# Performance work log

Hardware: AMD Instinct MI355X
Metric: run time of the kernel (lower is better)

Reference implementation:

```python
import jax, jax.numpy as jnp
import numpy as np

B, S, T = 32, 512, 2048
D_TXT, D_MEL = 256, 80


def conv1d(x, w, b, pad):
    # x: (B, C_in, L), w: (C_out, C_in, K)
    y = jax.lax.conv_general_dilated(x, w, window_strides=(1,), padding=[(pad, pad)],
                                     dimension_numbers=('NCH', 'OIH', 'NCH'))
    return y + b[None, :, None]


def text_encoder(x, tw1, tb1, tw2, tb2):
    h = jax.nn.relu(conv1d(x, tw1, tb1, 1))
    return conv1d(h, tw2, tb2, 0)


def mel_encoder(x, mw1, mb1, mw2, mb2, mw3, mb3):
    h = jax.nn.leaky_relu(conv1d(x, mw1, mb1, 1), 0.01)
    h = jax.nn.leaky_relu(conv1d(h, mw2, mb2, 1), 0.01)
    return conv1d(h, mw3, mb3, 0)


def cdist(a, b):
    # a: (B,S,D), b: (B,T,D) -> (B,S,T) euclidean (torch.cdist p=2)
    d2 = (jnp.sum(a * a, -1)[:, :, None] + jnp.sum(b * b, -1)[:, None, :]
          - 2.0 * jnp.einsum('bsd,btd->bst', a, b))
    return jnp.sqrt(jnp.maximum(d2, 1e-12))


def maximum_path(value, mask):
    # Glow-TTS monotonic alignment search. value, mask: (B,S,T) float.
    b, s, t = value.shape
    neg_inf = jnp.float32(-jnp.inf)
    val = (value * mask).transpose(2, 0, 1)  # (T,B,S)
    x_range = jnp.arange(s)

    def fwd_step(v, jc):
        j, col = jc
        v0 = jnp.concatenate([jnp.full((b, 1), neg_inf, v.dtype), v[:, :-1]], axis=1)
        keep = v >= v0  # True: best predecessor is same text index
        v_max = jnp.where(keep, v, v0)
        v_new = jnp.where(x_range[None, :] <= j, v_max + col, neg_inf)
        return v_new, keep

    _, dirs = jax.lax.scan(fwd_step, jnp.zeros((b, s), value.dtype), (jnp.arange(t), val))
    direction = jnp.where(mask.astype(bool), dirs.transpose(1, 2, 0), True).astype(jnp.int32)

    index0 = jnp.sum(mask[:, :, 0], axis=1).astype(jnp.int32) - 1

    def bwd_step(index, dcol):
        row = (jnp.arange(s)[None, :] == index[:, None]).astype(value.dtype)
        d = jnp.take_along_axis(dcol, index[:, None], axis=1)[:, 0]
        return index + d - 1, row

    dcols_rev = jnp.flip(direction, axis=2).transpose(2, 0, 1)  # (T,B,S)
    _, rows = jax.lax.scan(bwd_step, index0, dcols_rev)
    path = jnp.flip(rows, axis=0).transpose(1, 2, 0)  # (B,S,T)
    return path * mask


def setup_inputs() -> dict:
    key = jax.random.key(0)
    ks = jax.random.split(key, 16)
    text = jax.random.normal(ks[0], (B, S, D_TXT), jnp.float32)
    mel = jax.random.normal(ks[1], (B, T, D_MEL), jnp.float32)
    src_len = jax.random.randint(ks[2], (B,), S // 2, S + 1).astype(jnp.int32)
    mel_len = jax.random.randint(ks[3], (B,), T // 2, T + 1).astype(jnp.int32)
    src_mask = jnp.arange(S)[None, :] >= src_len[:, None]   # True = pad
    mel_mask = jnp.arange(T)[None, :] >= mel_len[:, None]
    attn_mask = jnp.zeros((B, S, T), bool)  # unused in forward
    sc = 0.05
    params = dict(
        tw1=jax.random.normal(ks[4], (512, 256, 3)) * sc, tb1=jnp.zeros((512,)),
        tw2=jax.random.normal(ks[5], (80, 512, 1)) * sc, tb2=jnp.zeros((80,)),
        mw1=jax.random.normal(ks[6], (160, 80, 3)) * sc, mb1=jnp.zeros((160,)),
        mw2=jax.random.normal(ks[7], (80, 160, 3)) * sc, mb2=jnp.zeros((80,)),
        mw3=jax.random.normal(ks[8], (80, 80, 1)) * sc, mb3=jnp.zeros((80,)),
    )
    return dict(text=text, mel=mel, src_len=src_len, mel_len=mel_len,
                src_mask=src_mask, mel_mask=mel_mask, attn_mask=attn_mask, **params)


def reference(text, mel, src_len, mel_len, src_mask, mel_mask, attn_mask,
              tw1, tb1, tw2, tb2, mw1, mb1, mw2, mb2, mw3, mb3):
    text_emb = text_encoder(text.transpose(0, 2, 1), tw1, tb1, tw2, tb2).transpose(0, 2, 1)
    mel_emb = mel_encoder(mel.transpose(0, 2, 1), mw1, mb1, mw2, mb2, mw3, mb3).transpose(0, 2, 1)
    text_emb = jnp.where(src_mask[:, :, None], 0.0, text_emb)
    mel_emb = jnp.where(mel_mask[:, :, None], 0.0, mel_emb)
    dist = cdist(text_emb, mel_emb)  # (B,S,T)
    mask1 = jnp.arange(S)[None, :] < src_len[:, None]
    mask2 = jnp.arange(T)[None, :] < mel_len[:, None]
    mask_ST = mask1[:, :, None] & mask2[:, None, :]
    rev = ~mask_ST
    logits = jnp.where(rev, jnp.float32(-1e9), -dist)
    soft_A = jax.nn.softmax(logits, axis=1)  # softmax over text dim
    soft_A = jnp.where(rev, 0.0, soft_A)
    hard_A = maximum_path(soft_A, mask_ST.astype(soft_A.dtype))
    return soft_A, hard_A, rev
```

## Files before the change

kernel.cpp:

```cpp
#include <hip/hip_runtime.h>
#include <hip/hip_bf16.h>
#include <cstdint>

constexpr int NB_ = 32;
constexpr int NS_ = 512;
constexpr int NT_ = 2048;
constexpr int DMEL = 80;

constexpr size_t P = 134217728ull;
constexpr size_t PO_TE   = 0ull;
constexpr size_t PO_ME   = 5242880ull;
constexpr size_t PO_NA   = 26214400ull;
constexpr size_t PO_NB   = 26279936ull;
constexpr size_t PO_W1   = 27066368ull;
constexpr size_t PO_W2   = 28639232ull;
constexpr size_t PO_W3   = 28803072ull;
constexpr size_t PO_W4   = 28956672ull;
constexpr size_t PO_W5   = 29110272ull;
constexpr size_t PO_DIR  = 29139968ull;
constexpr size_t FULL_NEED = P + 33334528ull;

__global__ void k_wtrans(const float* __restrict__ w, float* __restrict__ wT,
                         int CO, int CI, int KW, int total) {
  int id = blockIdx.x * 256 + threadIdx.x;
  if (id >= total) return;
  int co = id % CO;
  int rest = id / CO;
  int ci = rest % CI;
  int tap = rest / CI;
  wT[id] = w[(co * CI + ci) * KW + tap];
}

template <int CIN, int COUT, int NTILE, int NR, int KC, int LOG2L, int ACT,
          bool MASK, bool NORM>
__global__ __launch_bounds__(256) void k_conv(const float* __restrict__ x,
                                              const float* __restrict__ wT,
                                              const float* __restrict__ bias,
                                              float* __restrict__ y,
                                              const int* __restrict__ lenArr,
                                              float* __restrict__ normout) {
  constexpr int L = 1 << LOG2L;
  constexpr int MT = 128;
  constexpr int APAD = 132;
  constexpr int BPAD = NTILE + 4;
  __shared__ float As[KC][APAD];
  __shared__ float Bs[KC][BPAD];

  const int tid = threadIdx.x;
  const int tx = tid & 15;
  const int ty = tid >> 4;
  constexpr int NBLK = COUT / NTILE;
  const int m0 = (blockIdx.x / NBLK) * MT;
  const int n0 = (blockIdx.x % NBLK) * NTILE;

  float acc[8][NR];
#pragma unroll
  for (int i = 0; i < 8; ++i)
#pragma unroll
    for (int j = 0; j < NR; ++j) acc[i][j] = 0.f;

  for (int k0 = 0; k0 < CIN; k0 += KC) {
    __syncthreads();
    constexpr int AF4 = MT * KC / 4;
    constexpr int F4R = KC / 4;
    for (int f = tid; f < AF4; f += 256) {
      int row = f / F4R;
      int ko = (f % F4R) * 4;
      int r = m0 + row;
      float4 v = *reinterpret_cast<const float4*>(&x[(size_t)r * CIN + k0 + ko]);
      As[ko + 0][row] = v.x;
      As[ko + 1][row] = v.y;
      As[ko + 2][row] = v.z;
      As[ko + 3][row] = v.w;
    }
    constexpr int BF4 = KC * NTILE / 4;
    constexpr int BF4R = NTILE / 4;
    for (int f = tid; f < BF4; f += 256) {
      int kk = f / BF4R;
      int no = (f % BF4R) * 4;
      float4 v = *reinterpret_cast<const float4*>(
          &wT[((size_t)(k0 + kk)) * COUT + n0 + no]);
      *reinterpret_cast<float4*>(&Bs[kk][no]) = v;
    }
    __syncthreads();
#pragma unroll 8
    for (int kk = 0; kk < KC; ++kk) {
      float4 a0 = *reinterpret_cast<const float4*>(&As[kk][ty * 8]);
      float4 a1 = *reinterpret_cast<const float4*>(&As[kk][ty * 8 + 4]);
      float av[8] = {a0.x, a0.y, a0.z, a0.w, a1.x, a1.y, a1.z, a1.w};
      float bv[NR];
#pragma unroll
      for (int j = 0; j < NR; ++j) bv[j] = Bs[kk][tx * NR + j];
#pragma unroll
      for (int i = 0; i < 8; ++i)
#pragma unroll
        for (int j = 0; j < NR; ++j) acc[i][j] = fmaf(av[i], bv[j], acc[i][j]);
    }
  }
#pragma unroll
  for (int i = 0; i < 8; ++i) {
    int r = m0 + ty * 8 + i;
    int b = r >> LOG2L;
    int pos = r & (L - 1);
    bool zero = MASK && (pos >= lenArr[b]);
    float sq = 0.f;
#pragma unroll
    for (int j = 0; j < NR; ++j) {
      int c = n0 + tx * NR + j;
      float v = acc[i][j] + bias[c];
      if (ACT == 1) v = fmaxf(v, 0.f);
      if (ACT == 2) v = (v >= 0.f) ? v : 0.01f * v;
      if (zero) v = 0.f;
      y[(size_t)r * COUT + c] = v;
      if (NORM) sq = fmaf(v, v, sq);
    }
    if (NORM) {
      sq += __shfl_xor(sq, 1);
      sq += __shfl_xor(sq, 2);
      sq += __shfl_xor(sq, 4);
      sq += __shfl_xor(sq, 8);
      if (tx == 0) normout[r] = sq;
    }
  }
}

template <int CIN, int COUT, int NTILE, int NR, int KC, int LOG2L, int ACT>
__global__ __launch_bounds__(256) void k_conv3(const float* __restrict__ x,
                                               const float* __restrict__ wT,
                                               const float* __restrict__ bias,
                                               float* __restrict__ y) {
  constexpr int L = 1 << LOG2L;
  constexpr int MT = 128;
  constexpr int MT2 = MT + 2;
  constexpr int APAD = 132;
  constexpr int BPAD = NTILE + 4;
  __shared__ float As[KC][APAD];
  __shared__ float Bs[3][KC][BPAD];

  const int tid = threadIdx.x;
  const int tx = tid & 15;
  const int ty = tid >> 4;
  constexpr int NBLK = COUT / NTILE;
  const int m0 = (blockIdx.x / NBLK) * MT;
  const int n0 = (blockIdx.x % NBLK) * NTILE;
  const bool zlo = (m0 & (L - 1)) == 0;
  const bool zhi = ((m0 + MT) & (L - 1)) == 0;
  constexpr int TOTR = NB_ << LOG2L;

  float acc[8][NR];
#pragma unroll
  for (int i = 0; i < 8; ++i)
#pragma unroll
    for (int j = 0; j < NR; ++j) acc[i][j] = 0.f;

  for (int k0 = 0; k0 < CIN; k0 += KC) {
    __syncthreads();
    constexpr int F4R = KC / 4;
    for (int f = tid; f < MT2 * F4R; f += 256) {
      int h = f / F4R;
      int ko = (f % F4R) * 4;
      int g = m0 + h - 1;
      bool zero = (h == 0 && zlo) || (h == MT + 1 && zhi);
      int gc = g < 0 ? 0 : (g >= TOTR ? TOTR - 1 : g);
      float4 v = *reinterpret_cast<const float4*>(&x[(size_t)gc * CIN + k0 + ko]);
      if (zero) v = make_float4(0.f, 0.f, 0.f, 0.f);
      As[ko + 0][h] = v.x;
      As[ko + 1][h] = v.y;
      As[ko + 2][h] = v.z;
      As[ko + 3][h] = v.w;
    }
    constexpr int BF4R = NTILE / 4;
    for (int f = tid; f < 3 * KC * BF4R; f += 256) {
      int tap = f / (KC * BF4R);
      int rem = f % (KC * BF4R);
      int kk = rem / BF4R;
      int no = (rem % BF4R) * 4;
      float4 v = *reinterpret_cast<const float4*>(
          &wT[((size_t)(tap * CIN + k0 + kk)) * COUT + n0 + no]);
      *reinterpret_cast<float4*>(&Bs[tap][kk][no]) = v;
    }
    __syncthreads();
#pragma unroll 4
    for (int kk = 0; kk < KC; ++kk) {
      float aw[10];
      float4 a0 = *reinterpret_cast<const float4*>(&As[kk][ty * 8]);
      float4 a1 = *reinterpret_cast<const float4*>(&As[kk][ty * 8 + 4]);
      float2 a2 = *reinterpret_cast<const float2*>(&As[kk][ty * 8 + 8]);
      aw[0] = a0.x; aw[1] = a0.y; aw[2] = a0.z; aw[3] = a0.w;
      aw[4] = a1.x; aw[5] = a1.y; aw[6] = a1.z; aw[7] = a1.w;
      aw[8] = a2.x; aw[9] = a2.y;
#pragma unroll
      for (int tap = 0; tap < 3; ++tap) {
        float bv[NR];
#pragma unroll
        for (int j = 0; j < NR; ++j) bv[j] = Bs[tap][kk][tx * NR + j];
#pragma unroll
        for (int i = 0; i < 8; ++i)
#pragma unroll
          for (int j = 0; j < NR; ++j)
            acc[i][j] = fmaf(aw[i + tap], bv[j], acc[i][j]);
      }
    }
  }
#pragma unroll
  for (int i = 0; i < 8; ++i) {
    int r = m0 + ty * 8 + i;
#pragma unroll
    for (int j = 0; j < NR; ++j) {
      int c = n0 + tx * NR + j;
      float v = acc[i][j] + bias[c];
      if (ACT == 1) v = fmaxf(v, 0.f);
      if (ACT == 2) v = (v >= 0.f) ? v : 0.01f * v;
      y[(size_t)r * COUT + c] = v;
    }
  }
}

__global__ __launch_bounds__(256) void k_stats3(
    const float* __restrict__ te, const float* __restrict__ me,
    const float* __restrict__ na, const float* __restrict__ nb,
    const int* __restrict__ src_len, const int* __restrict__ mel_len,
    float* __restrict__ val, float* __restrict__ soft, float* __restrict__ rev) {
  const int b = blockIdx.x >> 5;
  const int t0 = (blockIdx.x & 31) << 6;
  const int sl = src_len[b], ml = mel_len[b];
  const int tid = threadIdx.x;
  const int lane = tid & 63, w = tid >> 6;

  if (t0 >= ml) {
    for (int c = 0; c < 8; ++c) {
      const int s0 = c << 6;
#pragma unroll 4
      for (int i = 0; i < 16; ++i) {
        const int s = s0 + (w << 4) + i;
        size_t o = ((size_t)b * NS_ + s) * NT_ + t0 + lane;
        soft[o] = 0.f;
        rev[o] = 1.f;
      }
    }
    return;
  }

  __shared__ float Bt[DMEL][68];
  __shared__ float At[DMEL][68];
  __shared__ float redm[16][64];
  __shared__ float redz[16][64];
  __shared__ float sm[64];
  __shared__ float srz[64];
  __shared__ float pl[64][65];
  for (int f = tid; f < 64 * 20; f += 256) {
    int row = f / 20, ko = (f % 20) << 2;
    float4 v = *reinterpret_cast<const float4*>(
        &me[((size_t)b * NT_ + t0 + row) * DMEL + ko]);
    Bt[ko][row] = v.x; Bt[ko + 1][row] = v.y; Bt[ko + 2][row] = v.z; Bt[ko + 3][row] = v.w;
  }
  const int sy = tid & 15, tx = tid >> 4;
  const float NEGINF = -__builtin_inff();
  float nbv[4], mACC[4], zACC[4];
#pragma unroll
  for (int j = 0; j < 4; ++j) {
    nbv[j] = nb[b * NT_ + t0 + (tx << 2) + j];
    mACC[j] = NEGINF;
    zACC[j] = 0.f;
  }
  for (int c = 0; c < 8; ++c) {
    const int s0 = c << 6;
    __syncthreads();
    for (int f = tid; f < 64 * 20; f += 256) {
      int row = f / 20, ko = (f % 20) << 2;
      float4 v = *reinterpret_cast<const float4*>(
          &te[((size_t)b * NS_ + s0 + row) * DMEL + ko]);
      At[ko][row] = v.x; At[ko + 1][row] = v.y; At[ko + 2][row] = v.z; At[ko + 3][row] = v.w;
    }
    __syncthreads();
    float acc[4][4];
#pragma unroll
    for (int i = 0; i < 4; ++i)
#pragma unroll
      for (int j = 0; j < 4; ++j) acc[i][j] = 0.f;
#pragma unroll 8
    for (int kk = 0; kk < DMEL; ++kk) {
      float4 a = *reinterpret_cast<const float4*>(&At[kk][sy << 2]);
      float4 bb = *reinterpret_cast<const float4*>(&Bt[kk][tx << 2]);
      float av[4] = {a.x, a.y, a.z, a.w}, bv[4] = {bb.x, bb.y, bb.z, bb.w};
#pragma unroll
      for (int i = 0; i < 4; ++i)
#pragma unroll
        for (int j = 0; j < 4; ++j) acc[i][j] = fmaf(av[i], bv[j], acc[i][j]);
    }
    float nav[4];
#pragma unroll
    for (int i = 0; i < 4; ++i) nav[i] = na[b * NS_ + s0 + (sy << 2) + i];
#pragma unroll
    for (int j = 0; j < 4; ++j) {
      const int t = t0 + (tx << 2) + j;
      const bool tvalid = t < ml;
      float ov[4];
      float mNew = mACC[j];
#pragma unroll
      for (int i = 0; i < 4; ++i) {
        float d2 = (nav[i] + nbv[j]) - 2.0f * acc[i][j];
        float dist = sqrtf(fmaxf(d2, 1e-12f));
        bool valid = ((s0 + (sy << 2) + i) < sl) && tvalid;
        ov[i] = valid ? -dist : -1e9f;
        mNew = fmaxf(mNew, ov[i]);
      }
      float scale = expf(mACC[j] - mNew);
      float zadd = 0.f;
#pragma unroll
      for (int i = 0; i < 4; ++i) zadd += expf(ov[i] - mNew);
      zACC[j] = zACC[j] * scale + zadd;
      mACC[j] = mNew;
      float4 o = make_float4(ov[0], ov[1], ov[2], ov[3]);
      *reinterpret_cast<float4*>(&val[((size_t)b * NT_ + t) * NS_ + s0 + (sy << 2)]) = o;
    }
  }
#pragma unroll
  for (int j = 0; j < 4; ++j) {
    redm[sy][(tx << 2) + j] = mACC[j];
    redz[sy][(tx << 2) + j] = zACC[j];
  }
  __syncthreads();
  if (tid < 64) {
    float M = NEGINF, Z = 0.f;
#pragma unroll
    for (int y = 0; y < 16; ++y) {
      float m = redm[y][tid], z = redz[y][tid];
      float Mn = fmaxf(M, m);
      Z = Z * expf(M - Mn) + z * expf(m - Mn);
      M = Mn;
    }
    sm[tid] = M;
    srz[tid] = 1.0f / Z;
  }
  __syncthreads();

  for (int c = 0; c < 8; ++c) {
    const int s0 = c << 6;
#pragma unroll
    for (int j = 0; j < 4; ++j) {
      const int tl = (tx << 2) + j;
      const int t = t0 + tl;
      const bool tvalid = t < ml;
      const float mv = sm[tl];
      const float rzv = srz[tl];
      float* vp = &val[((size_t)b * NT_ + t) * NS_ + s0 + (sy << 2)];
      float4 ov = *reinterpret_cast<const float4*>(vp);
      float4 p;
      p.x = tvalid ? expf(ov.x - mv) * rzv : 0.f;
      p.y = tvalid ? expf(ov.y - mv) * rzv : 0.f;
      p.z = tvalid ? expf(ov.z - mv) * rzv : 0.f;
      p.w = tvalid ? expf(ov.w - mv) * rzv : 0.f;
      *reinterpret_cast<float4*>(vp) = p;
      pl[tl][(sy << 2) + 0] = p.x;
      pl[tl][(sy << 2) + 1] = p.y;
      pl[tl][(sy << 2) + 2] = p.z;
      pl[tl][(sy << 2) + 3] = p.w;
    }
    __syncthreads();
#pragma unroll 4
    for (int i = 0; i < 16; ++i) {
      const int s_loc = (w << 4) + i;
      const int s = s0 + s_loc;
      float p = pl[lane][s_loc];
      size_t o = ((size_t)b * NS_ + s) * NT_ + t0 + lane;
      soft[o] = p;
      bool r = (s >= sl) || ((t0 + lane) >= ml);
      rev[o] = r ? 1.0f : 0.0f;
    }
    __syncthreads();
  }
}

__device__ __forceinline__ float dp_shr1(float x) {
  int r = __builtin_amdgcn_update_dpp(0, __float_as_int(x), 0x138, 0xF, 0xF, true);
  return __int_as_float(r);
}

__device__ __forceinline__ void dp_bar() {
  asm volatile("s_waitcnt lgkmcnt(0)" ::: "memory");
  __builtin_amdgcn_sched_barrier(0);
  __builtin_amdgcn_s_barrier();
}

#define DP_CHUNK(MASKED)                                                      \
  _Pragma("unroll")                                                           \
  for (int rb8 = 0; rb8 < 4; ++rb8) {                                         \
    float4 d0[4], d1[4];                                                      \
    _Pragma("unroll")                                                         \
    for (int rr = 0; rr < 4; ++rr) {                                          \
      const float* rp = rowbase + (((rb8 << 2) + rr) << 9);                   \
      d0[rr] = *reinterpret_cast<const float4*>(rp + (lane << 2));            \
      d1[rr] = *reinterpret_cast<const float4*>(rp + 256 + (lane << 2));      \
    }                                                                         \
    _Pragma("unroll")                                                         \
    for (int rr = 0; rr < 4; ++rr) {                                          \
      const int t = tbase + (rb8 << 2) + rr;                                  \
      float cc[8] = {d0[rr].x, d0[rr].y, d0[rr].z, d0[rr].w,                  \
                     d1[rr].x, d1[rr].y, d1[rr].z, d1[rr].w};                 \
      const int sh = t & 31;                                                  \
      if (t < ml) {                                                           \
        float up = dp_shr1(v[7]);                                             \
        float prev = (lane == 0) ? NEGINF : up;                               \
        _Pragma("unroll")                                                     \
        for (int j = 0; j < 8; ++j) {                                         \
          float cur = v[j];                                                   \
          bool keep = cur >= prev;                                            \
          float vm = fmaxf(cur, prev);                                        \
          float vn;                                                           \
          if (MASKED) {                                                       \
            int s = (lane << 3) + j;                                          \
            vn = (s <= t) ? vm + cc[j] : NEGINF;                              \
          } else {                                                            \
            vn = vm + cc[j];                                                  \
          }                                                                   \
          uint32_t bit = keep ? 1u : inv[j];                                  \
          bw[j] |= bit << sh;                                                 \
          v[j] = vn;                                                          \
          prev = cur;                                                         \
        }                                                                     \
      } else {                                                                \
        _Pragma("unroll")                                                     \
        for (int j = 0; j < 8; ++j) bw[j] |= 1u << sh;                        \
      }                                                                       \
    }                                                                         \
  }

__global__ __launch_bounds__(192) void k_dp(const float* __restrict__ val,
                                            const int* __restrict__ src_len,
                                            const int* __restrict__ mel_len,
                                            uint32_t* __restrict__ dir) {
  __shared__ float buf[2][16][512];
  const int b = blockIdx.x;
  const int wv = threadIdx.x >> 6;
  const int lane = threadIdx.x & 63;
  const float* base = val + (size_t)b * NT_ * NS_;
  const int sl = src_len[b];
  const int ml = mel_len[b];
  const float NEGINF = -__builtin_inff();
  int ca = ((ml + 31) >> 5) << 1;
  const int C_act = ca > 128 ? 128 : ca;

  float4 ra[8], rb[8];
  const int r0 = (wv - 1) << 3;

  float v[8];
  uint32_t bw[8], inv[8];
#pragma unroll
  for (int j = 0; j < 8; ++j) {
    v[j] = 0.0f;
    bw[j] = 0u;
    int s = (lane << 3) + j;
    inv[j] = (s < sl) ? 0u : 1u;
  }

  if (wv > 0) {
#pragma unroll
    for (int rr = 0; rr < 8; ++rr) {
      const float* g = base + (size_t)(r0 + rr) * NS_;
      ra[rr] = *reinterpret_cast<const float4*>(g + (lane << 3));
      rb[rr] = *reinterpret_cast<const float4*>(g + (lane << 3) + 4);
    }
#pragma unroll
    for (int rr = 0; rr < 8; ++rr) {
      float* l = &buf[0][r0 + rr][0];
      *reinterpret_cast<float4*>(l + (lane << 2)) = ra[rr];
      *reinterpret_cast<float4*>(l + 256 + (lane << 2)) = rb[rr];
    }
#pragma unroll
    for (int rr = 0; rr < 8; ++rr) {
      const float* g = base + (size_t)(16 + r0 + rr) * NS_;
      ra[rr] = *reinterpret_cast<const float4*>(g + (lane << 3));
      rb[rr] = *reinterpret_cast<const float4*>(g + (lane << 3) + 4);
    }
  }
  dp_bar();

  for (int c = 0; c < C_act; ++c) {
    if (wv > 0) {
      if (c + 1 < C_act) {
        const int nb = (c + 1) & 1;
#pragma unroll
        for (int rr = 0; rr < 8; ++rr) {
          float* l = &buf[nb][r0 + rr][0];
          *reinterpret_cast<float4*>(l + (lane << 2)) = ra[rr];
          *reinterpret_cast<float4*>(l + 256 + (lane << 2)) = rb[rr];
        }
      }
      if (c + 2 < C_act) {
        const float* cb = base + ((size_t)(c + 2) * 16 + r0) * NS_;
#pragma unroll
        for (int rr = 0; rr < 8; ++rr) {
          const float* g = cb + (size_t)rr * NS_;
          ra[rr] = *reinterpret_cast<const float4*>(g + (lane << 3));
          rb[rr] = *reinterpret_cast<const float4*>(g + (lane << 3) + 4);
        }
      }
    } else {
      const float* rowbase = &buf[c & 1][0][0];
      const int tbase = c << 4;
      if (c < 32) {
        DP_CHUNK(true)
      } else {
        DP_CHUNK(false)
      }
      if (c & 1) {
        const int c32 = c >> 1;
#pragma unroll
        for (int j = 0; j < 8; ++j) {
          dir[((size_t)(b * NS_) + (lane << 3) + j) * 64 + c32] = bw[j];
          bw[j] = 0u;
        }
      }
    }
    dp_bar();
  }
  if (wv == 0) {
    for (int c32 = C_act >> 1; c32 < 64; ++c32) {
#pragma unroll
      for (int j = 0; j < 8; ++j)
        dir[((size_t)(b * NS_) + (lane << 3) + j) * 64 + c32] = 0xFFFFFFFFu;
    }
  }
}

__global__ __launch_bounds__(256) void k_backtrack(
    const uint32_t* __restrict__ dir, const int* __restrict__ src_len,
    const int* __restrict__ mel_len, float* __restrict__ hard) {
  __shared__ uint32_t dl[NS_ * 64];
  const int b = blockIdx.x, tid = threadIdx.x;
  const uint32_t* db = dir + (size_t)b * NS_ * 64;
  for (int f = tid; f < 8192; f += 256) {
    int s = f >> 4;
    int wo = (f & 15) << 2;
    *reinterpret_cast<uint4*>(&dl[s * 64 + wo]) =
        *reinterpret_cast<const uint4*>(&db[s * 64 + wo]);
  }
  __syncthreads();
  if (tid == 0) {
    const int ml = mel_len[b];
    int idx = src_len[b] - 1;
    if (idx < 0) idx = 0;
    if (idx > NS_ - 1) idx = NS_ - 1;
    int cw = -1, ci = -1;
    uint32_t w = 0;
    for (int t = NT_ - 1; t >= 0; --t) {
      int wi = t >> 5;
      if (wi != cw || idx != ci) {
        w = dl[idx * 64 + wi];
        cw = wi;
        ci = idx;
      }
      if (t < ml) hard[((size_t)(b * NS_) + idx) * NT_ + t] = 1.0f;
      int step = (int)((w >> (t & 31)) & 1) - 1;
      idx += step;
      if (idx < 0) idx = 0;
    }
  }
}

extern "C" void kernel_launch(void* const* d_in, const int* in_sizes, int n_in,
                              void* d_out, int out_size, void* d_ws, size_t ws_size,
                              hipStream_t stream) {
  if (n_in != 17) return;
  if (ws_size < FULL_NEED) return;

  const float* text = (const float*)d_in[0];
  const float* mel = (const float*)d_in[1];
  const int* src_len = (const int*)d_in[2];
  const int* mel_len = (const int*)d_in[3];
  const float* tw1 = (const float*)d_in[7];
  const float* tb1 = (const float*)d_in[8];
  const float* tw2 = (const float*)d_in[9];
  const float* tb2 = (const float*)d_in[10];
  const float* mw1 = (const float*)d_in[11];
  const float* mb1 = (const float*)d_in[12];
  const float* mw2 = (const float*)d_in[13];
  const float* mb2 = (const float*)d_in[14];
  const float* mw3 = (const float*)d_in[15];
  const float* mb3 = (const float*)d_in[16];

  char* w8 = (char*)d_ws;
  float* melh1 = (float*)(w8 + 0);
  float* mh2 = (float*)(w8 + 41943040ull);
  float* texth1 = (float*)(w8 + 62914560ull);
  float* val = (float*)(w8 + 0);

  float* te = (float*)(w8 + P + PO_TE);
  float* me = (float*)(w8 + P + PO_ME);
  float* na = (float*)(w8 + P + PO_NA);
  float* nb = (float*)(w8 + P + PO_NB);
  float* wt1 = (float*)(w8 + P + PO_W1);
  float* wt2 = (float*)(w8 + P + PO_W2);
  float* wt3 = (float*)(w8 + P + PO_W3);
  float* wt4 = (float*)(w8 + P + PO_W4);
  float* wt5 = (float*)(w8 + P + PO_W5);
  uint32_t* dir = (uint32_t*)(w8 + P + PO_DIR);

  float* soft = (float*)d_out;
  float* hard = soft + (size_t)NB_ * NS_ * NT_;
  float* rev = soft + 2 * (size_t)NB_ * NS_ * NT_;

  k_wtrans<<<(512 * 256 * 3 + 255) / 256, 256, 0, stream>>>(tw1, wt1, 512, 256, 3, 512 * 256 * 3);
  k_wtrans<<<(80 * 512 + 255) / 256, 256, 0, stream>>>(tw2, wt2, 80, 512, 1, 80 * 512);
  k_wtrans<<<(160 * 80 * 3 + 255) / 256, 256, 0, stream>>>(mw1, wt3, 160, 80, 3, 160 * 80 * 3);
  k_wtrans<<<(80 * 160 * 3 + 255) / 256, 256, 0, stream>>>(mw2, wt4, 80, 160, 3, 80 * 160 * 3);
  k_wtrans<<<(80 * 80 + 255) / 256, 256, 0, stream>>>(mw3, wt5, 80, 80, 1, 80 * 80);

  k_conv3<80, 160, 80, 5, 16, 11, 2><<<512 * 2, 256, 0, stream>>>(mel, wt3, mb1, melh1);
  k_conv3<160, 80, 80, 5, 32, 11, 2><<<512 * 1, 256, 0, stream>>>(melh1, wt4, mb2, mh2);
  k_conv<80, 80, 80, 5, 16, 11, 0, true, true><<<512 * 1, 256, 0, stream>>>(mh2, wt5, mb3, me, mel_len, nb);
  k_conv3<256, 512, 128, 8, 32, 9, 1><<<128 * 4, 256, 0, stream>>>(text, wt1, tb1, texth1);
  k_conv<512, 80, 80, 5, 32, 9, 0, true, true><<<128 * 1, 256, 0, stream>>>(texth1, wt2, tb2, te, src_len, na);

  hipMemsetAsync(hard, 0, (size_t)NB_ * NS_ * NT_ * 4, stream);

  k_stats3<<<NB_ * 32, 256, 0, stream>>>(te, me, na, nb, src_len, mel_len, val, soft, rev);

  k_dp<<<NB_, 192, 0, stream>>>(val, src_len, mel_len, dir);
  k_backtrack<<<NB_, 256, 0, stream>>>(dir, src_len, mel_len, hard);
}
```

Before: 1.131 ms.

## Fuse backtrack into DP kernel and merge weight-transpose launches

Merges the five weight-transpose kernels into one launch that dispatches on the global thread index. Folds the backtracking pass into the end of the DP kernel, reusing its shared-memory buffer for the direction bits. Only the active direction words are loaded, the backtrack loop starts at mel_len instead of T, and the 0xFFFFFFFF fill of the unused direction words is dropped. This removes several kernel launches and redundant global traffic, but the DP kernel now needs a larger shared allocation and the backtrack runs in one thread of a 192-thread block.

```diff
diff --git a/kernel.cpp b/kernel.cpp
--- a/kernel.cpp
+++ b/kernel.cpp
@@ -20,15 +20,33 @@
 constexpr size_t PO_DIR  = 29139968ull;
 constexpr size_t FULL_NEED = P + 33334528ull;
 
-__global__ void k_wtrans(const float* __restrict__ w, float* __restrict__ wT,
-                         int CO, int CI, int KW, int total) {
+__global__ void k_wtrans_all(const float* __restrict__ w1, float* __restrict__ o1,
+                             const float* __restrict__ w2, float* __restrict__ o2,
+                             const float* __restrict__ w3, float* __restrict__ o3,
+                             const float* __restrict__ w4, float* __restrict__ o4,
+                             const float* __restrict__ w5, float* __restrict__ o5) {
   int id = blockIdx.x * 256 + threadIdx.x;
-  if (id >= total) return;
+  const float* w;
+  float* o;
+  int CO, CI, KW;
+  if (id < 393216) {
+    w = w1; o = o1; CO = 512; CI = 256; KW = 3;
+  } else if (id < 434176) {
+    id -= 393216; w = w2; o = o2; CO = 80; CI = 512; KW = 1;
+  } else if (id < 472576) {
+    id -= 434176; w = w3; o = o3; CO = 160; CI = 80; KW = 3;
+  } else if (id < 510976) {
+    id -= 472576; w = w4; o = o4; CO = 80; CI = 160; KW = 3;
+  } else if (id < 517376) {
+    id -= 510976; w = w5; o = o5; CO = 80; CI = 80; KW = 1;
+  } else {
+    return;
+  }
   int co = id % CO;
   int rest = id / CO;
   int ci = rest % CI;
   int tap = rest / CI;
-  wT[id] = w[(co * CI + ci) * KW + tap];
+  o[id] = w[(co * CI + ci) * KW + tap];
 }
 
 template <int CIN, int COUT, int NTILE, int NR, int KC, int LOG2L, int ACT,
@@ -383,6 +401,7 @@
   __builtin_amdgcn_s_barrier();
 }
 
+#define BUF(d, r, i) lbuf[(((d) << 4) + (r)) * 512 + (i)]
 #define DP_CHUNK(MASKED)                                                      \
   _Pragma("unroll")                                                           \
   for (int rb8 = 0; rb8 < 4; ++rb8) {                                         \
@@ -429,8 +448,10 @@
 __global__ __launch_bounds__(192) void k_dp(const float* __restrict__ val,
                                             const int* __restrict__ src_len,
                                             const int* __restrict__ mel_len,
-                                            uint32_t* __restrict__ dir) {
-  __shared__ float buf[2][16][512];
+                                            uint32_t* __restrict__ dir,
+                                            float* __restrict__ hard) {
+  __shared__ uint32_t smem[NS_ * 64];
+  float* lbuf = reinterpret_cast<float*>(smem);
   const int b = blockIdx.x;
   const int wv = threadIdx.x >> 6;
   const int lane = threadIdx.x & 63;
@@ -463,7 +484,7 @@
     }
 #pragma unroll
     for (int rr = 0; rr < 8; ++rr) {
-      float* l = &buf[0][r0 + rr][0];
+      float* l = &BUF(0, r0 + rr, 0);
       *reinterpret_cast<float4*>(l + (lane << 2)) = ra[rr];
       *reinterpret_cast<float4*>(l + 256 + (lane << 2)) = rb[rr];
     }
@@ -482,7 +503,7 @@
         const int nb = (c + 1) & 1;
 #pragma unroll
         for (int rr = 0; rr < 8; ++rr) {
-          float* l = &buf[nb][r0 + rr][0];
+          float* l = &BUF(nb, r0 + rr, 0);
           *reinterpret_cast<float4*>(l + (lane << 2)) = ra[rr];
           *reinterpret_cast<float4*>(l + 256 + (lane << 2)) = rb[rr];
         }
@@ -497,7 +518,7 @@
         }
       }
     } else {
-      const float* rowbase = &buf[c & 1][0][0];
+      const float* rowbase = &BUF(c & 1, 0, 0);
       const int tbase = c << 4;
       if (c < 32) {
         DP_CHUNK(true)
@@ -515,43 +536,31 @@
     }
     dp_bar();
   }
-  if (wv == 0) {
-    for (int c32 = C_act >> 1; c32 < 64; ++c32) {
-#pragma unroll
-      for (int j = 0; j < 8; ++j)
-        dir[((size_t)(b * NS_) + (lane << 3) + j) * 64 + c32] = 0xFFFFFFFFu;
-    }
-  }
-}
-
-__global__ __launch_bounds__(256) void k_backtrack(
-    const uint32_t* __restrict__ dir, const int* __restrict__ src_len,
-    const int* __restrict__ mel_len, float* __restrict__ hard) {
-  __shared__ uint32_t dl[NS_ * 64];
-  const int b = blockIdx.x, tid = threadIdx.x;
+
+  __syncthreads();
+  const int tid = threadIdx.x;
   const uint32_t* db = dir + (size_t)b * NS_ * 64;
-  for (int f = tid; f < 8192; f += 256) {
-    int s = f >> 4;
-    int wo = (f & 15) << 2;
-    *reinterpret_cast<uint4*>(&dl[s * 64 + wo]) =
-        *reinterpret_cast<const uint4*>(&db[s * 64 + wo]);
+  const int wlim = C_act >> 1;
+  for (int f = tid; f < NS_ * wlim; f += 192) {
+    int s = f / wlim;
+    int wi = f - s * wlim;
+    smem[s * 64 + wi] = db[s * 64 + wi];
   }
   __syncthreads();
   if (tid == 0) {
-    const int ml = mel_len[b];
-    int idx = src_len[b] - 1;
+    int idx = sl - 1;
     if (idx < 0) idx = 0;
     if (idx > NS_ - 1) idx = NS_ - 1;
     int cw = -1, ci = -1;
     uint32_t w = 0;
-    for (int t = NT_ - 1; t >= 0; --t) {
+    for (int t = ml - 1; t >= 0; --t) {
       int wi = t >> 5;
       if (wi != cw || idx != ci) {
-        w = dl[idx * 64 + wi];
+        w = smem[idx * 64 + wi];
         cw = wi;
         ci = idx;
       }
-      if (t < ml) hard[((size_t)(b * NS_) + idx) * NT_ + t] = 1.0f;
+      hard[((size_t)(b * NS_) + idx) * NT_ + t] = 1.0f;
       int step = (int)((w >> (t & 31)) & 1) - 1;
       idx += step;
       if (idx < 0) idx = 0;
@@ -601,11 +610,8 @@
   float* hard = soft + (size_t)NB_ * NS_ * NT_;
   float* rev = soft + 2 * (size_t)NB_ * NS_ * NT_;
 
-  k_wtrans<<<(512 * 256 * 3 + 255) / 256, 256, 0, stream>>>(tw1, wt1, 512, 256, 3, 512 * 256 * 3);
-  k_wtrans<<<(80 * 512 + 255) / 256, 256, 0, stream>>>(tw2, wt2, 80, 512, 1, 80 * 512);
-  k_wtrans<<<(160 * 80 * 3 + 255) / 256, 256, 0, stream>>>(mw1, wt3, 160, 80, 3, 160 * 80 * 3);
-  k_wtrans<<<(80 * 160 * 3 + 255) / 256, 256, 0, stream>>>(mw2, wt4, 80, 160, 3, 80 * 160 * 3);
-  k_wtrans<<<(80 * 80 + 255) / 256, 256, 0, stream>>>(mw3, wt5, 80, 80, 1, 80 * 80);
+  k_wtrans_all<<<(517376 + 255) / 256, 256, 0, stream>>>(
+      tw1, wt1, tw2, wt2, mw1, wt3, mw2, wt4, mw3, wt5);
 
   k_conv3<80, 160, 80, 5, 16, 11, 2><<<512 * 2, 256, 0, stream>>>(mel, wt3, mb1, melh1);
   k_conv3<160, 80, 80, 5, 32, 11, 2><<<512 * 1, 256, 0, stream>>>(melh1, wt4, mb2, mh2);
@@ -617,6 +623,5 @@
 
   k_stats3<<<NB_ * 32, 256, 0, stream>>>(te, me, na, nb, src_len, mel_len, val, soft, rev);
 
-  k_dp<<<NB_, 192, 0, stream>>>(val, src_len, mel_len, dir);
-  k_backtrack<<<NB_, 256, 0, stream>>>(dir, src_len, mel_len, hard);
-}
+  k_dp<<<NB_, 192, 0, stream>>>(val, src_len, mel_len, dir, hard);
+}
```

Measured after the change: 1.114 ms. Within noise of the previous version (-1.5%).
